# Performance work log

Hardware: AMD Instinct MI355X
Metric: run time of the kernel (lower is better)

Reference implementation:

```python
import jax, jax.numpy as jnp
import numpy as np

B, S, DIM = 2, 2048, 2048
NH, NKV = 16, 16
HD = 128            # constructor head_dim (full per-head dim, = 2 * self.head_dim)
HHD = HD // 2       # self.head_dim = per-stream dim = 64
ROPE_THETA = 10000.0
LAMBDA_INIT = 0.8 - 0.6 * float(np.exp(-0.3 * 0))  # block_id = 0 -> 0.2
EPS = 1e-5


def make_freq_cis(seq_len, dim, theta):
    # rotation matrices, shape (seq, dim//2, 2, 2): [[cos, -sin], [sin, cos]]
    inv = 1.0 / (theta ** (np.arange(0, dim, 2, dtype=np.float32) / dim))
    ang = np.arange(seq_len, dtype=np.float32)[:, None] * inv[None, :]
    cos, sin = np.cos(ang), np.sin(ang)
    fc = np.stack([np.stack([cos, -sin], -1), np.stack([sin, cos], -1)], -2)
    return jnp.asarray(fc, dtype=jnp.float32)


def setup_inputs() -> dict:
    key = jax.random.key(0)
    ks = jax.random.split(key, 9)
    std = DIM ** -0.5
    return {
        "x": jax.random.normal(ks[0], (B, S, DIM), jnp.float32),
        "freq_cis": make_freq_cis(S, HD, ROPE_THETA),
        "wq": jax.random.normal(ks[1], (NH * HD, DIM), jnp.float32) * std,
        "wk": jax.random.normal(ks[2], (NKV * HD, DIM), jnp.float32) * std,
        "wv": jax.random.normal(ks[3], (NKV * HD, DIM), jnp.float32) * std,
        "wo": jax.random.normal(ks[4], (DIM, NH * HD), jnp.float32) * std,
        "lambda_q1": jax.random.normal(ks[5], (HHD,), jnp.float32) * 0.1,
        "lambda_k1": jax.random.normal(ks[6], (HHD,), jnp.float32) * 0.1,
        "lambda_q2": jax.random.normal(ks[7], (HHD,), jnp.float32) * 0.1,
        "lambda_k2": jax.random.normal(ks[8], (HHD,), jnp.float32) * 0.1,
        "subln_w": jnp.ones((HD,), jnp.float32),
    }


def _rope(t, fc):
    # t: (b, s, h, d); fc: (s, d//2, 2, 2). Pairs (even, odd) rotated by 2x2 matrix.
    b, s, h, d = t.shape
    t2 = t.reshape(b, s, h, d // 2, 1, 2)
    out = (t2 * fc[None, :, None]).sum(-1)  # (b, s, h, d//2, 2)
    return out.reshape(b, s, h, d)


def _causal_attn(q, k, v):
    # q, k: (b, s, h, HHD); v: (b, s, h, HD). Flash-attn default scale = 1/sqrt(q head dim).
    scale = 1.0 / jnp.sqrt(jnp.asarray(q.shape[-1], q.dtype))
    scores = jnp.einsum('bqhd,bkhd->bhqk', q, k) * scale
    s = q.shape[1]
    causal = jnp.tril(jnp.ones((s, s), bool))
    scores = jnp.where(causal, scores, jnp.finfo(scores.dtype).min)
    p = jax.nn.softmax(scores, axis=-1)
    return jnp.einsum('bhqk,bkhd->bqhd', p, v)  # (b, s, h, HD)


def reference(x, freq_cis, wq, wk, wv, wo, lambda_q1, lambda_k1, lambda_q2, lambda_k2, subln_w):
    b, s, _ = x.shape
    xq = (x @ wq.T).reshape(b, s, NH, HD)
    xk = (x @ wk.T).reshape(b, s, NKV, HD)
    xv = (x @ wv.T).reshape(b, s, NKV, HD)
    xq = _rope(xq, freq_cis)
    xk = _rope(xk, freq_cis)
    if NKV != NH:  # GQA: repeat kv heads group-wise
        rep = NH // NKV
        xk = jnp.repeat(xk, rep, axis=2)
        xv = jnp.repeat(xv, rep, axis=2)
    # split each head into two differential streams of size HHD
    xq = xq.reshape(b, s, NH, 2, HHD)
    xk = xk.reshape(b, s, NH, 2, HHD)
    attn1 = _causal_attn(xq[:, :, :, 0], xk[:, :, :, 0], xv)
    attn2 = _causal_attn(xq[:, :, :, 1], xk[:, :, :, 1], xv)
    lam1 = jnp.exp(jnp.sum(lambda_q1 * lambda_k1))
    lam2 = jnp.exp(jnp.sum(lambda_q2 * lambda_k2))
    lam_full = lam1 - lam2 + LAMBDA_INIT
    attn = attn1 - lam_full * attn2              # (b, s, h, HD)
    attn = jnp.transpose(attn, (0, 2, 1, 3))     # faithful to torch .transpose(1, 2)
    ms = jnp.mean(jnp.square(attn), axis=-1, keepdims=True)
    attn = attn * jax.lax.rsqrt(ms + EPS) * subln_w  # RMSNorm(2*HHD)
    attn = attn * (1.0 - LAMBDA_INIT)
    # faithful to original: reshape (b, h, s, HD) row-major into (b, s, h*HD)
    attn = attn.reshape(b, s, NH * HD)
    return attn @ wo.T
```

## Files before the change

### kernel.cpp

```cpp
#include <hip/hip_runtime.h>

typedef unsigned short u16;
typedef unsigned int   u32;
typedef __attribute__((ext_vector_type(8))) short s16x8;
typedef __attribute__((ext_vector_type(4))) float f32x4;

constexpr int Bc = 2, Sc = 2048, DIMc = 2048, NHc = 16, HDc = 128, Tc = Bc * Sc;
constexpr float LAMBDA_INIT_C = 0.2f;

__device__ __forceinline__ u16 f2bf(float f) {
  union { float f; u32 u; } v; v.f = f;
  u32 r = v.u + 0x7fffu + ((v.u >> 16) & 1u);
  return (u16)(r >> 16);
}
__device__ __forceinline__ float bf2f(u16 b) {
  union { u32 u; float f; } v; v.u = ((u32)b) << 16;
  return v.f;
}
__device__ __forceinline__ f32x4 mfma16(s16x8 a, s16x8 b, f32x4 c) {
  return __builtin_amdgcn_mfma_f32_16x16x32_bf16(a, b, c, 0, 0, 0);
}

typedef const __attribute__((address_space(1))) u32 gq32;
typedef __attribute__((address_space(3))) u32 lq32;
__device__ __forceinline__ void cp16(const u16* g, u16* l) {
  __builtin_amdgcn_global_load_lds((gq32*)g, (lq32*)l, 16, 0, 0);
}

__global__ void cvt_kernel(const float* __restrict__ src, u16* __restrict__ dst, int n4) {
  int i = blockIdx.x * 256 + threadIdx.x;
  if (i >= n4) return;
  const float4 v = ((const float4*)src)[i];
  union { u16 u[4]; uint2 p; } o;
  o.u[0] = f2bf(v.x); o.u[1] = f2bf(v.y); o.u[2] = f2bf(v.z); o.u[3] = f2bf(v.w);
  ((uint2*)dst)[i] = o.p;
}

__global__ void cvt4_kernel(const float* __restrict__ s0, const float* __restrict__ s1,
                            const float* __restrict__ s2, const float* __restrict__ s3,
                            u16* __restrict__ dst) {
  const int per = DIMc * DIMc / 4;
  int i = blockIdx.x * 256 + threadIdx.x;
  const int which = i / per, j = i - which * per;
  const float* src = which == 0 ? s0 : which == 1 ? s1 : which == 2 ? s2 : s3;
  const float4 v = ((const float4*)src)[j];
  union { u16 u[4]; uint2 p; } o;
  o.u[0] = f2bf(v.x); o.u[1] = f2bf(v.y); o.u[2] = f2bf(v.z); o.u[3] = f2bf(v.w);
  ((uint2*)dst)[i] = o.p;
}

__global__ __launch_bounds__(256) void gemm_qkv(const u16* __restrict__ A,
                                                const u16* __restrict__ Wq,
                                                const u16* __restrict__ Wk,
                                                const u16* __restrict__ Wv,
                                                u16* __restrict__ Oq,
                                                u16* __restrict__ Ok,
                                                u16* __restrict__ Ov) {
  constexpr int K = DIMc, N = DIMc;
  __shared__ u16 lA[128 * 32];
  __shared__ u16 lB[128 * 32];
  const int nglob = blockIdx.x * 128;
  const int which = nglob >> 11;
  const u16* Bw = which == 0 ? Wq : which == 1 ? Wk : Wv;
  u16*       Cb = which == 0 ? Oq : which == 1 ? Ok : Ov;
  const int nbase = nglob & (N - 1);
  const int mbase = blockIdx.y * 128;

  const int tid  = threadIdx.x;
  const int lane = tid & 63;
  const int w    = tid >> 6;
  const int wrow = (w >> 1) * 64;
  const int wcol = (w & 1) * 64;
  const int l15  = lane & 15;
  const int quad = lane >> 4;

  f32x4 acc[4][4];
#pragma unroll
  for (int i = 0; i < 4; i++)
#pragma unroll
    for (int j = 0; j < 4; j++) acc[i][j] = (f32x4){0.f, 0.f, 0.f, 0.f};

  const int srow = w * 32 + (lane >> 2);
  const int scol = (lane & 3) * 8;
  const u16* gA = A  + (size_t)(mbase + srow) * K + scol;
  const u16* gB = Bw + (size_t)(nbase + srow) * K + scol;
  u16* sA = lA + srow * 32 + scol;
  u16* sB = lB + srow * 32 + scol;

  for (int kb = 0; kb < K; kb += 32) {
    __syncthreads();
    cp16(gA + kb,                  sA);
    cp16(gA + kb + (size_t)16 * K, sA + 16 * 32);
    cp16(gB + kb,                  sB);
    cp16(gB + kb + (size_t)16 * K, sB + 16 * 32);
    __syncthreads();
    s16x8 af[4], bfr[4];
#pragma unroll
    for (int i = 0; i < 4; i++)
      af[i] = *(const s16x8*)(lA + (wrow + i * 16 + l15) * 32 + quad * 8);
#pragma unroll
    for (int j = 0; j < 4; j++)
      bfr[j] = *(const s16x8*)(lB + (wcol + j * 16 + l15) * 32 + quad * 8);
#pragma unroll
    for (int i = 0; i < 4; i++)
#pragma unroll
      for (int j = 0; j < 4; j++) acc[i][j] = mfma16(af[i], bfr[j], acc[i][j]);
  }

#pragma unroll
  for (int i = 0; i < 4; i++) {
    const int m0 = mbase + wrow + i * 16 + quad * 4;
#pragma unroll
    for (int j = 0; j < 4; j++) {
      const int n0 = nbase + wcol + j * 16 + l15;
#pragma unroll
      for (int r = 0; r < 4; r++) Cb[(size_t)(m0 + r) * N + n0] = f2bf(acc[i][j][r]);
    }
  }
}

__global__ __launch_bounds__(256) void gemm_bt(const u16* __restrict__ A,
                                               const u16* __restrict__ Bw,
                                               float* __restrict__ Cf,
                                               int M, int N, int K) {
  __shared__ u16 lA[128 * 32];
  __shared__ u16 lB[128 * 32];
  const int tid  = threadIdx.x;
  const int lane = tid & 63;
  const int w    = tid >> 6;
  const int mbase = blockIdx.y * 128;
  const int nbase = blockIdx.x * 128;
  const int wrow = (w >> 1) * 64;
  const int wcol = (w & 1) * 64;
  const int l15  = lane & 15;
  const int quad = lane >> 4;

  f32x4 acc[4][4];
#pragma unroll
  for (int i = 0; i < 4; i++)
#pragma unroll
    for (int j = 0; j < 4; j++) acc[i][j] = (f32x4){0.f, 0.f, 0.f, 0.f};

  const int srow = w * 32 + (lane >> 2);
  const int scol = (lane & 3) * 8;
  const u16* gA = A  + (size_t)(mbase + srow) * K + scol;
  const u16* gB = Bw + (size_t)(nbase + srow) * K + scol;
  u16* sA = lA + srow * 32 + scol;
  u16* sB = lB + srow * 32 + scol;

  for (int kb = 0; kb < K; kb += 32) {
    __syncthreads();
    cp16(gA + kb,                  sA);
    cp16(gA + kb + (size_t)16 * K, sA + 16 * 32);
    cp16(gB + kb,                  sB);
    cp16(gB + kb + (size_t)16 * K, sB + 16 * 32);
    __syncthreads();
    s16x8 af[4], bfr[4];
#pragma unroll
    for (int i = 0; i < 4; i++)
      af[i] = *(const s16x8*)(lA + (wrow + i * 16 + l15) * 32 + quad * 8);
#pragma unroll
    for (int j = 0; j < 4; j++)
      bfr[j] = *(const s16x8*)(lB + (wcol + j * 16 + l15) * 32 + quad * 8);
#pragma unroll
    for (int i = 0; i < 4; i++)
#pragma unroll
      for (int j = 0; j < 4; j++) acc[i][j] = mfma16(af[i], bfr[j], acc[i][j]);
  }

#pragma unroll
  for (int i = 0; i < 4; i++) {
    const int m0 = mbase + wrow + i * 16 + quad * 4;
#pragma unroll
    for (int j = 0; j < 4; j++) {
      const int n0 = nbase + wcol + j * 16 + l15;
#pragma unroll
      for (int r = 0; r < 4; r++) Cf[(size_t)(m0 + r) * N + n0] = acc[i][j][r];
    }
  }
}

__global__ void rope_kernel(const u16* __restrict__ xg, const float* __restrict__ fc,
                            u16* __restrict__ out, float scale) {
  const int idx = blockIdx.x * 256 + threadIdx.x;
  const int p = idx & 63;
  const int h = (idx >> 6) & 15;
  const int t = idx >> 10;
  const int s = t & (Sc - 1);
  const int b = t >> 11;
  const float c  = fc[(size_t)(s * 64 + p) * 4 + 0] * scale;
  const float sn = fc[(size_t)(s * 64 + p) * 4 + 2] * scale;
  const u16* px = xg + (size_t)t * DIMc + h * HDc + p * 2;
  const float x0 = bf2f(px[0]), x1 = bf2f(px[1]);
  u16* po = out + ((size_t)(b * NHc + h) * Sc + s) * HDc + p * 2;
  po[0] = f2bf(c * x0 - sn * x1);
  po[1] = f2bf(sn * x0 + c * x1);
}

__global__ void vtrans_kernel(const u16* __restrict__ vg, u16* __restrict__ vt) {
  __shared__ u16 tile[32][33];
  const int bh = blockIdx.z;
  const int b = bh >> 4, h = bh & 15;
  const int s0 = blockIdx.x * 32, d0 = blockIdx.y * 32;
  const int tx = threadIdx.x & 31, ty = threadIdx.x >> 5;
#pragma unroll
  for (int pp = 0; pp < 4; pp++) {
    const int s = s0 + ty + pp * 8;
    tile[ty + pp * 8][tx] = vg[(size_t)(b * Sc + s) * DIMc + h * HDc + d0 + tx];
  }
  __syncthreads();
#pragma unroll
  for (int pp = 0; pp < 4; pp++) {
    const int d = d0 + ty + pp * 8;
    vt[((size_t)bh * HDc + d) * Sc + s0 + tx] = tile[tx][ty + pp * 8];
  }
}

__global__ __launch_bounds__(256, 2) void diff_attn_kernel(
    const u16* __restrict__ qr, const u16* __restrict__ kr, const u16* __restrict__ vt,
    const float* __restrict__ lq1, const float* __restrict__ lk1,
    const float* __restrict__ lq2, const float* __restrict__ lk2,
    const float* __restrict__ subw, u16* __restrict__ Y) {
  __shared__ u16 KB[2][4096];
  __shared__ u16 VB[2][4096];
  __shared__ float SB[4][2][16 * 36];

  const int h = blockIdx.y, b = blockIdx.z, jb = blockIdx.x;
  const int bh = b * NHc + h;
  const int tid = threadIdx.x;
  const int w = tid >> 6, lane = tid & 63;
  const int l15 = lane & 15, quad = lane >> 4;

  const u16* krb = kr + (size_t)bh * Sc * HDc;
  const u16* vtb = vt + (size_t)bh * HDc * Sc;

  float lp1 = lq1[lane] * lk1[lane];
  float lp2 = lq2[lane] * lk2[lane];
#pragma unroll
  for (int m = 32; m; m >>= 1) { lp1 += __shfl_xor(lp1, m); lp2 += __shfl_xor(lp2, m); }
  const float lam = __expf(lp1) - __expf(lp2) + LAMBDA_INIT_C;

  float wsub[8];
#pragma unroll
  for (int dn = 0; dn < 8; dn++) wsub[dn] = subw[dn * 16 + l15];

  float* sbS[2] = { SB[w][0], SB[w][1] };

  for (int ph = 0; ph < 2; ph++) {
    const int t = ph ? (31 - jb) : jb;
    const int rowbase = t * 64 + w * 16;
    const int nc = 2 * t + 2;

    const u16* qp = qr + ((size_t)bh * Sc + rowbase + l15) * HDc + quad * 8;
    s16x8 qa[2][2];
    qa[0][0] = *(const s16x8*)(qp);
    qa[0][1] = *(const s16x8*)(qp + 32);
    qa[1][0] = *(const s16x8*)(qp + 64);
    qa[1][1] = *(const s16x8*)(qp + 96);

    f32x4 o[2][8];
#pragma unroll
    for (int st = 0; st < 2; st++)
#pragma unroll
      for (int dn = 0; dn < 8; dn++) o[st][dn] = (f32x4){0.f, 0.f, 0.f, 0.f};
    float lpart[2] = { 0.f, 0.f };

    __syncthreads();
    {
#pragma unroll
      for (int oo = 0; oo < 2; oo++) {
        const int n = (2 * w + oo) * 64 + lane;
        cp16(krb + (size_t)(n & 31) * HDc + (n >> 5) * 8, KB[0] + n * 8);
      }
#pragma unroll
      for (int oo = 0; oo < 2; oo++) {
        const int n = (2 * w + oo) * 64 + lane;
        cp16(vtb + (size_t)(n & 127) * Sc + (n >> 7) * 8, VB[0] + n * 8);
      }
    }

    for (int c = 0; c < nc; c++) {
      __syncthreads();
      if (c + 1 < nc) {
        const int kb1 = (c + 1) * 32;
        u16* Kn = KB[(c + 1) & 1];
        u16* Vn = VB[(c + 1) & 1];
#pragma unroll
        for (int oo = 0; oo < 2; oo++) {
          const int n = (2 * w + oo) * 64 + lane;
          cp16(krb + (size_t)(kb1 + (n & 31)) * HDc + (n >> 5) * 8, Kn + n * 8);
        }
#pragma unroll
        for (int oo = 0; oo < 2; oo++) {
          const int n = (2 * w + oo) * 64 + lane;
          cp16(vtb + (size_t)(n & 127) * Sc + kb1 + (n >> 7) * 8, Vn + n * 8);
        }
      }
      const u16* Kb = KB[c & 1];
      const u16* Vb = VB[c & 1];
      const int kb = c * 32;

      f32x4 sc[2][2];
#pragma unroll
      for (int st = 0; st < 2; st++)
#pragma unroll
        for (int kt = 0; kt < 2; kt++) sc[st][kt] = (f32x4){0.f, 0.f, 0.f, 0.f};
#pragma unroll
      for (int st = 0; st < 2; st++)
#pragma unroll
        for (int kh = 0; kh < 2; kh++) {
          const int dblk = st * 8 + kh * 4 + quad;
#pragma unroll
          for (int kt = 0; kt < 2; kt++) {
            const s16x8 kf = *(const s16x8*)(Kb + ((size_t)dblk * 32 + kt * 16 + l15) * 8);
            sc[st][kt] = mfma16(qa[st][kh], kf, sc[st][kt]);
          }
        }

#pragma unroll
      for (int st = 0; st < 2; st++)
#pragma unroll
        for (int kt = 0; kt < 2; kt++)
#pragma unroll
          for (int r = 0; r < 4; r++)
            sbS[st][(quad * 4 + r) * 36 + kt * 16 + l15] = sc[st][kt][r];

      s16x8 pa[2];
      const bool diag = (c >= nc - 2);
#pragma unroll
      for (int st = 0; st < 2; st++) {
        const float* sb = sbS[st];
        const float4 u0 = *(const float4*)(sb + l15 * 36 + quad * 8);
        const float4 u1 = *(const float4*)(sb + l15 * 36 + quad * 8 + 4);
        float v[8] = { u0.x, u0.y, u0.z, u0.w, u1.x, u1.y, u1.z, u1.w };
        float p[8], sm = 0.f;
#pragma unroll
        for (int j8 = 0; j8 < 8; j8++) p[j8] = __expf(v[j8]);
        if (diag) {
          const int qrow = rowbase + l15;
#pragma unroll
          for (int j8 = 0; j8 < 8; j8++)
            if (kb + quad * 8 + j8 > qrow) p[j8] = 0.f;
        }
#pragma unroll
        for (int j8 = 0; j8 < 8; j8++) sm += p[j8];
        lpart[st] += sm;
        union { u16 us[8]; s16x8 vv; } pk;
#pragma unroll
        for (int j8 = 0; j8 < 8; j8++) pk.us[j8] = f2bf(p[j8]);
        pa[st] = pk.vv;
      }

#pragma unroll
      for (int dn = 0; dn < 8; dn++) {
        const s16x8 vf = *(const s16x8*)(Vb + ((size_t)quad * 128 + dn * 16 + l15) * 8);
        o[0][dn] = mfma16(pa[0], vf, o[0][dn]);
        o[1][dn] = mfma16(pa[1], vf, o[1][dn]);
      }
    }

    float lL0 = lpart[0], lL1 = lpart[1];
    lL0 += __shfl_xor(lL0, 16); lL0 += __shfl_xor(lL0, 32);
    lL1 += __shfl_xor(lL1, 16); lL1 += __shfl_xor(lL1, 32);
    const float inv1 = 1.f / lL0;
    const float inv2 = lam / lL1;
    float i1C[4], i2C[4];
#pragma unroll
    for (int r = 0; r < 4; r++) {
      i1C[r] = __shfl(inv1, quad * 4 + r, 16);
      i2C[r] = __shfl(inv2, quad * 4 + r, 16);
    }
    float yv[8][4], ss[4] = { 0.f, 0.f, 0.f, 0.f };
#pragma unroll
    for (int dn = 0; dn < 8; dn++)
#pragma unroll
      for (int r = 0; r < 4; r++) {
        const float y = o[0][dn][r] * i1C[r] - o[1][dn][r] * i2C[r];
        yv[dn][r] = y;
        ss[r] += y * y;
      }
#pragma unroll
    for (int r = 0; r < 4; r++) {
#pragma unroll
      for (int mm = 1; mm < 16; mm <<= 1) ss[r] += __shfl_xor(ss[r], mm);
    }
    float scl[4];
#pragma unroll
    for (int r = 0; r < 4; r++) scl[r] = rsqrtf(ss[r] * (1.f / 128.f) + 1e-5f) * 0.8f;

    u16* yrow = Y + ((size_t)(b * Sc + h * 128 + t * 4 + w)) * 2048;
#pragma unroll
    for (int dn = 0; dn < 8; dn++)
#pragma unroll
      for (int r = 0; r < 4; r++)
        yrow[(quad * 4 + r) * 128 + dn * 16 + l15] = f2bf(yv[dn][r] * scl[r] * wsub[dn]);
  }
}

extern "C" void kernel_launch(void* const* d_in, const int* in_sizes, int n_in,
                              void* d_out, int out_size, void* d_ws, size_t ws_size,
                              hipStream_t stream) {
  const float* x    = (const float*)d_in[0];
  const float* fc   = (const float*)d_in[1];
  const float* wq   = (const float*)d_in[2];
  const float* wk   = (const float*)d_in[3];
  const float* wv   = (const float*)d_in[4];
  const float* wo   = (const float*)d_in[5];
  const float* lq1  = (const float*)d_in[6];
  const float* lk1  = (const float*)d_in[7];
  const float* lq2  = (const float*)d_in[8];
  const float* lk2  = (const float*)d_in[9];
  const float* subw = (const float*)d_in[10];
  float* out = (float*)d_out;

  char* ws = (char*)d_ws;
  constexpr size_t SZ_X  = (size_t)Tc * DIMc * 2;
  constexpr size_t SZ_W  = (size_t)DIMc * DIMc * 2;
  constexpr size_t SZ_T  = (size_t)Tc * DIMc * 2;
  u16* xb  = (u16*)(ws);
  u16* wqb = (u16*)(ws + SZ_X);
  u16* wkb = (u16*)(ws + SZ_X + SZ_W);
  u16* wvb = (u16*)(ws + SZ_X + 2 * SZ_W);
  u16* wob = (u16*)(ws + SZ_X + 3 * SZ_W);
  u16* qg  = (u16*)(ws + SZ_X + 4 * SZ_W);
  u16* kg  = (u16*)(ws + SZ_X + 4 * SZ_W + SZ_T);
  u16* vg  = (u16*)(ws + SZ_X + 4 * SZ_W + 2 * SZ_T);
  u16* qr  = (u16*)(ws + SZ_X + 4 * SZ_W + 3 * SZ_T);
  u16* kr  = (u16*)(ws + SZ_X + 4 * SZ_W + 4 * SZ_T);
  u16* vt  = (u16*)(ws + SZ_X + 4 * SZ_W + 5 * SZ_T);
  u16* Y   = (u16*)(ws + SZ_X + 4 * SZ_W + 6 * SZ_T);

  cvt_kernel<<<(Tc * DIMc / 4 + 255) / 256, 256, 0, stream>>>(x, xb, Tc * DIMc / 4);
  cvt4_kernel<<<4 * (DIMc * DIMc / 4) / 256, 256, 0, stream>>>(wq, wk, wv, wo, wqb);

  gemm_qkv<<<dim3(48, Tc / 128), 256, 0, stream>>>(xb, wqb, wkb, wvb, qg, kg, vg);

  const int ropeBlocks = Tc * NHc * 64 / 256;
  rope_kernel<<<ropeBlocks, 256, 0, stream>>>(qg, fc, qr, 0.125f);
  rope_kernel<<<ropeBlocks, 256, 0, stream>>>(kg, fc, kr, 1.0f);
  vtrans_kernel<<<dim3(Sc / 32, HDc / 32, Bc * NHc), 256, 0, stream>>>(vg, vt);

  diff_attn_kernel<<<dim3(16, NHc, Bc), 256, 0, stream>>>(
      qr, kr, vt, lq1, lk1, lq2, lk2, subw, Y);

  gemm_bt<<<dim3(DIMc / 128, Tc / 128), 256, 0, stream>>>(Y, wob, out, Tc, DIMc, DIMc);
}
```

Before: 471.0 us.

## Widen attention key tiles, drop LDS score shuffle, fuse prep and convert kernels

The attention kernel now processes 64-key chunks per iteration, with K rows permuted on load and QK^T computed transposed. Each lane's MFMA output then lines up directly with the P operand layout, so the LDS round-trip for scores goes away and half the barriers per key range are removed. Fully masked sub-tiles on the diagonal are skipped for half the waves. Separately, the input/weight conversion kernels are merged into one launch, and the two rope launches plus the V transpose are merged into one prep kernel with packed 32-bit loads and stores. LDS usage doubles per block, which may affect occupancy.

Result: faster. 437.9 us (-7.0%).

```diff
diff --git a/kernel.cpp b/kernel.cpp
--- a/kernel.cpp
+++ b/kernel.cpp
@@ -27,26 +27,28 @@
   __builtin_amdgcn_global_load_lds((gq32*)g, (lq32*)l, 16, 0, 0);
 }
 
-__global__ void cvt_kernel(const float* __restrict__ src, u16* __restrict__ dst, int n4) {
-  int i = blockIdx.x * 256 + threadIdx.x;
-  if (i >= n4) return;
-  const float4 v = ((const float4*)src)[i];
+__global__ void cvt_all_kernel(const float* __restrict__ x,
+                               const float* __restrict__ wq, const float* __restrict__ wk,
+                               const float* __restrict__ wv, const float* __restrict__ wo,
+                               u16* __restrict__ xb, u16* __restrict__ wb) {
+  const int i = blockIdx.x * 256 + threadIdx.x;
+  constexpr int NX = Tc * DIMc / 4;
+  constexpr int PW = DIMc * DIMc / 4;
+  float4 v; uint2* dst;
+  if (i < NX) {
+    v = ((const float4*)x)[i];
+    dst = ((uint2*)xb) + i;
+  } else {
+    const int j = i - NX;
+    const int which = j >> 20;
+    const int jj = j & (PW - 1);
+    const float* src = which == 0 ? wq : which == 1 ? wk : which == 2 ? wv : wo;
+    v = ((const float4*)src)[jj];
+    dst = ((uint2*)wb) + j;
+  }
   union { u16 u[4]; uint2 p; } o;
   o.u[0] = f2bf(v.x); o.u[1] = f2bf(v.y); o.u[2] = f2bf(v.z); o.u[3] = f2bf(v.w);
-  ((uint2*)dst)[i] = o.p;
-}
-
-__global__ void cvt4_kernel(const float* __restrict__ s0, const float* __restrict__ s1,
-                            const float* __restrict__ s2, const float* __restrict__ s3,
-                            u16* __restrict__ dst) {
-  const int per = DIMc * DIMc / 4;
-  int i = blockIdx.x * 256 + threadIdx.x;
-  const int which = i / per, j = i - which * per;
-  const float* src = which == 0 ? s0 : which == 1 ? s1 : which == 2 ? s2 : s3;
-  const float4 v = ((const float4*)src)[j];
-  union { u16 u[4]; uint2 p; } o;
-  o.u[0] = f2bf(v.x); o.u[1] = f2bf(v.y); o.u[2] = f2bf(v.z); o.u[3] = f2bf(v.w);
-  ((uint2*)dst)[i] = o.p;
+  *dst = o.p;
 }
 
 __global__ __launch_bounds__(256) void gemm_qkv(const u16* __restrict__ A,
@@ -180,39 +182,49 @@
   }
 }
 
-__global__ void rope_kernel(const u16* __restrict__ xg, const float* __restrict__ fc,
-                            u16* __restrict__ out, float scale) {
-  const int idx = blockIdx.x * 256 + threadIdx.x;
-  const int p = idx & 63;
-  const int h = (idx >> 6) & 15;
-  const int t = idx >> 10;
-  const int s = t & (Sc - 1);
-  const int b = t >> 11;
-  const float c  = fc[(size_t)(s * 64 + p) * 4 + 0] * scale;
-  const float sn = fc[(size_t)(s * 64 + p) * 4 + 2] * scale;
-  const u16* px = xg + (size_t)t * DIMc + h * HDc + p * 2;
-  const float x0 = bf2f(px[0]), x1 = bf2f(px[1]);
-  u16* po = out + ((size_t)(b * NHc + h) * Sc + s) * HDc + p * 2;
-  po[0] = f2bf(c * x0 - sn * x1);
-  po[1] = f2bf(sn * x0 + c * x1);
-}
-
-__global__ void vtrans_kernel(const u16* __restrict__ vg, u16* __restrict__ vt) {
+__global__ void prep_kernel(const u16* __restrict__ qg, const u16* __restrict__ kg,
+                            const u16* __restrict__ vg, const float* __restrict__ fc,
+                            u16* __restrict__ qr, u16* __restrict__ kr,
+                            u16* __restrict__ vt) {
   __shared__ u16 tile[32][33];
-  const int bh = blockIdx.z;
-  const int b = bh >> 4, h = bh & 15;
-  const int s0 = blockIdx.x * 32, d0 = blockIdx.y * 32;
-  const int tx = threadIdx.x & 31, ty = threadIdx.x >> 5;
-#pragma unroll
-  for (int pp = 0; pp < 4; pp++) {
-    const int s = s0 + ty + pp * 8;
-    tile[ty + pp * 8][tx] = vg[(size_t)(b * Sc + s) * DIMc + h * HDc + d0 + tx];
-  }
-  __syncthreads();
-#pragma unroll
-  for (int pp = 0; pp < 4; pp++) {
-    const int d = d0 + ty + pp * 8;
-    vt[((size_t)bh * HDc + d) * Sc + s0 + tx] = tile[tx][ty + pp * 8];
+  const int bid = blockIdx.x;
+  if (bid < 32768) {
+    const bool isq = bid < 16384;
+    const u16* xg = isq ? qg : kg;
+    u16* outp = isq ? qr : kr;
+    const float scale = isq ? 0.125f : 1.0f;
+    const int idx = (bid & 16383) * 256 + threadIdx.x;
+    const int p = idx & 63;
+    const int hh = (idx >> 6) & 15;
+    const int tt = idx >> 10;
+    const int s = tt & (Sc - 1);
+    const int bb = tt >> 11;
+    const float c  = fc[(size_t)(s * 64 + p) * 4 + 0] * scale;
+    const float sn = fc[(size_t)(s * 64 + p) * 4 + 2] * scale;
+    const u32 xp = *(const u32*)(xg + (size_t)tt * DIMc + hh * HDc + p * 2);
+    const float x0 = bf2f((u16)xp), x1 = bf2f((u16)(xp >> 16));
+    const u16 y0 = f2bf(c * x0 - sn * x1);
+    const u16 y1 = f2bf(sn * x0 + c * x1);
+    *(u32*)(outp + ((size_t)(bb * NHc + hh) * Sc + s) * HDc + p * 2) =
+        (u32)y0 | ((u32)y1 << 16);
+  } else {
+    const int vb = bid - 32768;
+    const int bh = vb >> 8;
+    const int bb = bh >> 4, hh = bh & 15;
+    const int rem = vb & 255;
+    const int s0 = (rem & 63) * 32, d0 = (rem >> 6) * 32;
+    const int tx = threadIdx.x & 31, ty = threadIdx.x >> 5;
+#pragma unroll
+    for (int pp = 0; pp < 4; pp++) {
+      const int s = s0 + ty + pp * 8;
+      tile[ty + pp * 8][tx] = vg[(size_t)(bb * Sc + s) * DIMc + hh * HDc + d0 + tx];
+    }
+    __syncthreads();
+#pragma unroll
+    for (int pp = 0; pp < 4; pp++) {
+      const int d = d0 + ty + pp * 8;
+      vt[((size_t)bh * HDc + d) * Sc + s0 + tx] = tile[tx][ty + pp * 8];
+    }
   }
 }
 
@@ -221,9 +233,8 @@
     const float* __restrict__ lq1, const float* __restrict__ lk1,
     const float* __restrict__ lq2, const float* __restrict__ lk2,
     const float* __restrict__ subw, u16* __restrict__ Y) {
-  __shared__ u16 KB[2][4096];
-  __shared__ u16 VB[2][4096];
-  __shared__ float SB[4][2][16 * 36];
+  __shared__ u16 KB[2][8192];
+  __shared__ u16 VB[2][8192];
 
   const int h = blockIdx.y, b = blockIdx.z, jb = blockIdx.x;
   const int bh = b * NHc + h;
@@ -244,12 +255,22 @@
 #pragma unroll
   for (int dn = 0; dn < 8; dn++) wsub[dn] = subw[dn * 16 + l15];
 
-  float* sbS[2] = { SB[w][0], SB[w][1] };
+  size_t offK[4], offV[4];
+  int dstO[4];
+#pragma unroll
+  for (int oo = 0; oo < 4; oo++) {
+    const int n = w * 256 + oo * 64 + lane;
+    const int s = n & 31, dblk = (n >> 5) & 15, sub = n >> 9;
+    const int mkey = (s & 3) + ((s >> 2) & 3) * 8 + ((s >> 4) << 2);
+    offK[oo] = (size_t)(sub * 32 + mkey) * HDc + dblk * 8;
+    offV[oo] = (size_t)(n & 127) * Sc + (sub * 32 + ((n >> 7) & 3) * 8);
+    dstO[oo] = n * 8;
+  }
 
   for (int ph = 0; ph < 2; ph++) {
     const int t = ph ? (31 - jb) : jb;
     const int rowbase = t * 64 + w * 16;
-    const int nc = 2 * t + 2;
+    const int nc = t + 1;
 
     const u16* qp = qr + ((size_t)bh * Sc + rowbase + l15) * HDc + quad * 8;
     s16x8 qa[2][2];
@@ -266,96 +287,80 @@
     float lpart[2] = { 0.f, 0.f };
 
     __syncthreads();
-    {
-#pragma unroll
-      for (int oo = 0; oo < 2; oo++) {
-        const int n = (2 * w + oo) * 64 + lane;
-        cp16(krb + (size_t)(n & 31) * HDc + (n >> 5) * 8, KB[0] + n * 8);
-      }
-#pragma unroll
-      for (int oo = 0; oo < 2; oo++) {
-        const int n = (2 * w + oo) * 64 + lane;
-        cp16(vtb + (size_t)(n & 127) * Sc + (n >> 7) * 8, VB[0] + n * 8);
-      }
-    }
+#pragma unroll
+    for (int oo = 0; oo < 4; oo++) cp16(krb + offK[oo], KB[0] + dstO[oo]);
+#pragma unroll
+    for (int oo = 0; oo < 4; oo++) cp16(vtb + offV[oo], VB[0] + dstO[oo]);
 
     for (int c = 0; c < nc; c++) {
       __syncthreads();
       if (c + 1 < nc) {
-        const int kb1 = (c + 1) * 32;
+        const int kb1 = (c + 1) * 64;
         u16* Kn = KB[(c + 1) & 1];
         u16* Vn = VB[(c + 1) & 1];
 #pragma unroll
-        for (int oo = 0; oo < 2; oo++) {
-          const int n = (2 * w + oo) * 64 + lane;
-          cp16(krb + (size_t)(kb1 + (n & 31)) * HDc + (n >> 5) * 8, Kn + n * 8);
-        }
-#pragma unroll
-        for (int oo = 0; oo < 2; oo++) {
-          const int n = (2 * w + oo) * 64 + lane;
-          cp16(vtb + (size_t)(n & 127) * Sc + kb1 + (n >> 7) * 8, Vn + n * 8);
-        }
+        for (int oo = 0; oo < 4; oo++) cp16(krb + (size_t)kb1 * HDc + offK[oo], Kn + dstO[oo]);
+#pragma unroll
+        for (int oo = 0; oo < 4; oo++) cp16(vtb + offV[oo] + kb1, Vn + dstO[oo]);
       }
       const u16* Kb = KB[c & 1];
       const u16* Vb = VB[c & 1];
-      const int kb = c * 32;
-
-      f32x4 sc[2][2];
-#pragma unroll
-      for (int st = 0; st < 2; st++)
-#pragma unroll
-        for (int kt = 0; kt < 2; kt++) sc[st][kt] = (f32x4){0.f, 0.f, 0.f, 0.f};
-#pragma unroll
-      for (int st = 0; st < 2; st++)
-#pragma unroll
-        for (int kh = 0; kh < 2; kh++) {
-          const int dblk = st * 8 + kh * 4 + quad;
-#pragma unroll
-          for (int kt = 0; kt < 2; kt++) {
-            const s16x8 kf = *(const s16x8*)(Kb + ((size_t)dblk * 32 + kt * 16 + l15) * 8);
-            sc[st][kt] = mfma16(qa[st][kh], kf, sc[st][kt]);
+      const int kb = c * 64;
+      const bool diag = (c == nc - 1);
+
+#pragma unroll
+      for (int sub = 0; sub < 2; sub++) {
+        if (diag && sub == 1 && w < 2) continue;
+
+        f32x4 sc[2][2];
+#pragma unroll
+        for (int st = 0; st < 2; st++)
+#pragma unroll
+          for (int kt = 0; kt < 2; kt++) sc[st][kt] = (f32x4){0.f, 0.f, 0.f, 0.f};
+#pragma unroll
+        for (int st = 0; st < 2; st++)
+#pragma unroll
+          for (int kh = 0; kh < 2; kh++) {
+            const int base = sub * 512 + (st * 8 + kh * 4 + quad) * 32;
+#pragma unroll
+            for (int kt = 0; kt < 2; kt++) {
+              const s16x8 kf = *(const s16x8*)(Kb + (size_t)(base + kt * 16 + l15) * 8);
+              sc[st][kt] = mfma16(kf, qa[st][kh], sc[st][kt]);
+            }
           }
+
+        s16x8 pa[2];
+#pragma unroll
+        for (int st = 0; st < 2; st++) {
+          float p[8];
+#pragma unroll
+          for (int kt = 0; kt < 2; kt++)
+#pragma unroll
+            for (int r = 0; r < 4; r++) p[kt * 4 + r] = __expf(sc[st][kt][r]);
+          if (diag) {
+            const int qrow = rowbase + l15;
+            const int kb0 = kb + sub * 32 + quad * 8;
+#pragma unroll
+            for (int j8 = 0; j8 < 8; j8++)
+              if (kb0 + j8 > qrow) p[j8] = 0.f;
+          }
+          float sm = 0.f;
+#pragma unroll
+          for (int j8 = 0; j8 < 8; j8++) sm += p[j8];
+          lpart[st] += sm;
+          union { u16 us[8]; s16x8 vv; } pk;
+#pragma unroll
+          for (int j8 = 0; j8 < 8; j8++) pk.us[j8] = f2bf(p[j8]);
+          pa[st] = pk.vv;
         }
 
 #pragma unroll
-      for (int st = 0; st < 2; st++)
-#pragma unroll
-        for (int kt = 0; kt < 2; kt++)
-#pragma unroll
-          for (int r = 0; r < 4; r++)
-            sbS[st][(quad * 4 + r) * 36 + kt * 16 + l15] = sc[st][kt][r];
-
-      s16x8 pa[2];
-      const bool diag = (c >= nc - 2);
-#pragma unroll
-      for (int st = 0; st < 2; st++) {
-        const float* sb = sbS[st];
-        const float4 u0 = *(const float4*)(sb + l15 * 36 + quad * 8);
-        const float4 u1 = *(const float4*)(sb + l15 * 36 + quad * 8 + 4);
-        float v[8] = { u0.x, u0.y, u0.z, u0.w, u1.x, u1.y, u1.z, u1.w };
-        float p[8], sm = 0.f;
-#pragma unroll
-        for (int j8 = 0; j8 < 8; j8++) p[j8] = __expf(v[j8]);
-        if (diag) {
-          const int qrow = rowbase + l15;
-#pragma unroll
-          for (int j8 = 0; j8 < 8; j8++)
-            if (kb + quad * 8 + j8 > qrow) p[j8] = 0.f;
+        for (int dn = 0; dn < 8; dn++) {
+          const s16x8 vf =
+              *(const s16x8*)(Vb + (size_t)(sub * 512 + quad * 128 + dn * 16 + l15) * 8);
+          o[0][dn] = mfma16(pa[0], vf, o[0][dn]);
+          o[1][dn] = mfma16(pa[1], vf, o[1][dn]);
         }
-#pragma unroll
-        for (int j8 = 0; j8 < 8; j8++) sm += p[j8];
-        lpart[st] += sm;
-        union { u16 us[8]; s16x8 vv; } pk;
-#pragma unroll
-        for (int j8 = 0; j8 < 8; j8++) pk.us[j8] = f2bf(p[j8]);
-        pa[st] = pk.vv;
-      }
-
-#pragma unroll
-      for (int dn = 0; dn < 8; dn++) {
-        const s16x8 vf = *(const s16x8*)(Vb + ((size_t)quad * 128 + dn * 16 + l15) * 8);
-        o[0][dn] = mfma16(pa[0], vf, o[0][dn]);
-        o[1][dn] = mfma16(pa[1], vf, o[1][dn]);
       }
     }
 
@@ -430,15 +435,12 @@
   u16* vt  = (u16*)(ws + SZ_X + 4 * SZ_W + 5 * SZ_T);
   u16* Y   = (u16*)(ws + SZ_X + 4 * SZ_W + 6 * SZ_T);
 
-  cvt_kernel<<<(Tc * DIMc / 4 + 255) / 256, 256, 0, stream>>>(x, xb, Tc * DIMc / 4);
-  cvt4_kernel<<<4 * (DIMc * DIMc / 4) / 256, 256, 0, stream>>>(wq, wk, wv, wo, wqb);
+  cvt_all_kernel<<<(Tc * DIMc / 4 + 4 * DIMc * DIMc / 4) / 256, 256, 0, stream>>>(
+      x, wq, wk, wv, wo, xb, wqb);
 
   gemm_qkv<<<dim3(48, Tc / 128), 256, 0, stream>>>(xb, wqb, wkb, wvb, qg, kg, vg);
 
-  const int ropeBlocks = Tc * NHc * 64 / 256;
-  rope_kernel<<<ropeBlocks, 256, 0, stream>>>(qg, fc, qr, 0.125f);
-  rope_kernel<<<ropeBlocks, 256, 0, stream>>>(kg, fc, kr, 1.0f);
-  vtrans_kernel<<<dim3(Sc / 32, HDc / 32, Bc * NHc), 256, 0, stream>>>(vg, vt);
+  prep_kernel<<<16384 + 16384 + 8192, 256, 0, stream>>>(qg, kg, vg, fc, qr, kr, vt);
 
   diff_attn_kernel<<<dim3(16, NHc, Bc), 256, 0, stream>>>(
       qr, kr, vt, lq1, lk1, lq2, lk2, subw, Y);
```
